# Kernel optimization log

Measured on AMD Instinct MI355X. Metric: run time of the kernel, lower is better.

## Reference

```python
import jax, jax.numpy as jnp
import numpy as np

B, N, FD = 2, 50000, 13
E = 250000
M, H = 128, 128          # message_dim, hidden_dim
EDGE_IN = 2 * FD + 8     # 34
NODE_IN = FD + 2 * M     # 269


def _mlp(x, w1, b1, w2, b2):
    return jnp.tanh(x @ w1 + b1) @ w2 + b2


def setup_inputs() -> dict:
    root = jax.random.key(0)
    k = lambda i: jax.random.fold_in(root, i)

    def lin(i, din, dout):
        w = jax.random.normal(k(i), (din, dout), jnp.float32) * np.float32(1.0 / np.sqrt(din))
        b = jax.random.normal(k(i + 100), (dout,), jnp.float32) * np.float32(0.01)
        return w, b

    ew1, eb1 = lin(1, EDGE_IN, H); ew2, eb2 = lin(2, H, M)      # mlp_edge
    ww1, wb1 = lin(3, EDGE_IN, H); ww2, wb2 = lin(4, H, 1)      # mlp_weight
    xw1, xb1 = lin(5, EDGE_IN, H); xw2, xb2 = lin(6, H, M)      # mlp_edge_world
    yw1, yb1 = lin(7, EDGE_IN, H); yw2, yb2 = lin(8, H, 1)      # mlp_weight_world
    nw1, nb1 = lin(9, NODE_IN, H); nw2, nb2 = lin(10, H, FD)    # mlp_node

    z_h = jax.random.normal(k(20), (B, N, FD), jnp.float32)
    edge_hh = jax.random.randint(k(21), (B, 2, E), 0, N, jnp.int32)
    edge_world = jax.random.randint(k(22), (B, 2, E), 0, N, jnp.int32)
    return dict(z_h=z_h, edge_hh=edge_hh, edge_world=edge_world,
                ew1=ew1, eb1=eb1, ew2=ew2, eb2=eb2,
                ww1=ww1, wb1=wb1, ww2=ww2, wb2=wb2,
                xw1=xw1, xb1=xb1, xw2=xw2, xb2=xb2,
                yw1=yw1, yb1=yb1, yw2=yw2, yb2=yb2,
                nw1=nw1, nb1=nb1, nw2=nw2, nb2=nb2)


def _edge_features(z, s, t):
    # z: (N, FD); s, t: (E,)
    pos, vel = z[:, 0:3], z[:, 3:6]
    diff = pos[s] - pos[t]                               # (E, 3)
    dist = jnp.sum(diff * diff, axis=-1, keepdims=True)  # (E, 1) squared distance
    vxc = jnp.cross(vel[s], vel[t])                      # (E, 3)
    vxn = jnp.linalg.norm(vxc, axis=-1, keepdims=True)   # (E, 1)
    return jnp.concatenate([diff, dist, vxc, vxn], axis=-1)  # (E, 8)


def reference(z_h, edge_hh, edge_world,
              ew1, eb1, ew2, eb2, ww1, wb1, ww2, wb2,
              xw1, xb1, xw2, xb2, yw1, yb1, yw2, yb2,
              nw1, nb1, nw2, nb2):
    n_nodes = z_h.shape[1]

    def per_batch(z, e_hh, e_w):
        # normal edges
        s, t = e_hh[0], e_hh[1]
        inp = jnp.concatenate([z[s], z[t], _edge_features(z, s, t)], axis=-1)  # (E, 34)
        m = _mlp(inp, ew1, eb1, ew2, eb2)                                       # (E, M)
        w = jax.nn.sigmoid(_mlp(inp, ww1, wb1, ww2, wb2))                       # (E, 1)
        agg_h = jnp.zeros((n_nodes, M), z.dtype).at[t].add(w * m)
        # world edges
        sw, tw = e_w[0], e_w[1]
        inpw = jnp.concatenate([z[sw], z[tw], _edge_features(z, sw, tw)], axis=-1)
        mw = _mlp(inpw, xw1, xb1, xw2, xb2)
        ww_ = jax.nn.sigmoid(_mlp(inpw, yw1, yb1, yw2, yb2))
        agg_w = jnp.zeros((n_nodes, M), z.dtype).at[tw].add(ww_ * mw)
        return agg_h, agg_w

    m_agg_h, m_agg_w = jax.vmap(per_batch)(z_h, edge_hh, edge_world)  # (B, N, M) each
    input_node = jnp.concatenate([z_h, m_agg_h, m_agg_w], axis=-1)    # (B, N, 269)
    delta_z_h = _mlp(input_node, nw1, nb1, nw2, nb2)                  # (B, N, 13)
    return delta_z_h
```

## Files before the change

### kernel.cpp

```cpp
#include <hip/hip_runtime.h>
#include <hip/hip_bf16.h>

#define B_   2
#define N_   50000
#define FD_  13
#define E_   250000
#define M_   128
#define H_   128

typedef __attribute__((ext_vector_type(8))) short  short8;
typedef __attribute__((ext_vector_type(8))) __bf16 bf16x8;
typedef __attribute__((ext_vector_type(4))) float  f32x4;
typedef __attribute__((ext_vector_type(4))) unsigned int uint4v;
typedef __attribute__((ext_vector_type(8))) unsigned short ushort8;

#define AGG_BYTES  (4ull * N_ * 128 * 4)
#define HIST_BYTES (4ull * N_ * 4)
#define SORT_BYTES (4ull * E_ * 4)
#define OFF_EW1 0u
#define OFF_WW1 8192u
#define OFF_EW2 16384u
#define OFF_XW1 32768u
#define OFF_YW1 40960u
#define OFF_XW2 49152u
#define OFF_NW1 65536u
#define OFF_NW2 102400u

__device__ __forceinline__ float bf2f(unsigned short u) {
    unsigned int v = ((unsigned int)u) << 16;
    return __builtin_bit_cast(float, v);
}
__device__ __forceinline__ unsigned short f2bf(float f) {
    __bf16 h = (__bf16)f;
    return __builtin_bit_cast(unsigned short, h);
}
__device__ __forceinline__ float tanh_fast(float x) {
    float e = __expf(x + x);
    float r = __builtin_amdgcn_rcpf(e + 1.0f);
    return __builtin_fmaf(-2.0f, r, 1.0f);
}
__device__ __forceinline__ float sigmoid_fast(float x) {
    return __builtin_amdgcn_rcpf(1.0f + __expf(-x));
}
__device__ __forceinline__ f32x4 mfma16(short8 a, short8 b, f32x4 c) {
    return __builtin_amdgcn_mfma_f32_16x16x32_bf16(
        __builtin_bit_cast(bf16x8, a), __builtin_bit_cast(bf16x8, b), c, 0, 0, 0);
}

__global__ void prep_kernel(const float* __restrict__ ew1, const float* __restrict__ ww1,
                            const float* __restrict__ ew2, const float* __restrict__ xw1,
                            const float* __restrict__ yw1, const float* __restrict__ xw2,
                            const float* __restrict__ nw1, const float* __restrict__ nw2,
                            unsigned short* __restrict__ fb, uint4v* __restrict__ hist4) {
    int m = blockIdx.y, f = blockIdx.x, l = threadIdx.x;
    {
        unsigned int flat = ((unsigned int)m * gridDim.x + (unsigned int)f) * 64u + (unsigned int)l;
        const uint4v zv = {0u, 0u, 0u, 0u};
        for (unsigned int i = flat; i < 50000u; i += gridDim.x * gridDim.y * 64u)
            hist4[i] = zv;
    }
    const float* src; int K, Nn, KS; unsigned int off;
    switch (m) {
        case 0: src = ew1; K = 34;  Nn = 128; KS = 2; off = OFF_EW1; break;
        case 1: src = ww1; K = 34;  Nn = 128; KS = 2; off = OFF_WW1; break;
        case 2: src = ew2; K = 128; Nn = 128; KS = 4; off = OFF_EW2; break;
        case 3: src = xw1; K = 34;  Nn = 128; KS = 2; off = OFF_XW1; break;
        case 4: src = yw1; K = 34;  Nn = 128; KS = 2; off = OFF_YW1; break;
        case 5: src = xw2; K = 128; Nn = 128; KS = 4; off = OFF_XW2; break;
        case 6: src = nw1; K = 269; Nn = 128; KS = 9; off = OFF_NW1; break;
        default: src = nw2; K = 128; Nn = 13; KS = 4; off = OFF_NW2; break;
    }
    int NT = (Nn + 15) / 16;
    if (f >= KS * NT) return;
    int ks = f / NT, nt = f % NT;
    int n = nt * 16 + (l & 15);
    unsigned short* dst = fb + off + ((unsigned int)f * 64u + (unsigned int)l) * 8u;
    #pragma unroll
    for (int j = 0; j < 8; j++) {
        int k = ks * 32 + ((l >> 4) * 8) + j;
        int kk = k; bool valid = (k < K) && (n < Nn);
        if (m == 6) {
            if (k < 256)      kk = k + 13;
            else if (k < 269) kk = k - 256;
            else              valid = false;
            valid = valid && (n < Nn);
        }
        dst[j] = valid ? f2bf(src[kk * Nn + n]) : (unsigned short)0;
    }
}

__global__ void hist_kernel(const int* __restrict__ ehh, const int* __restrict__ eww,
                            int* __restrict__ hist) {
    int p = blockIdx.y, idx = blockIdx.x * 256 + threadIdx.x;
    if (idx >= E_) return;
    const int* eg = ((p >> 1) ? eww : ehh) + (size_t)(p & 1) * 2 * E_;
    atomicAdd(&hist[p * N_ + eg[E_ + idx]], 1);
}

__global__ void scan_kernel(int* __restrict__ hist) {
    __shared__ int part[1024];
    const int p = blockIdx.x, tid = threadIdx.x;
    int* h = hist + p * N_;
    const int lo = tid * 52;
    int cnt = N_ - lo; if (cnt < 0) cnt = 0; if (cnt > 52) cnt = 52;
    int v[52];
    int sum = 0;
    if (cnt == 52) {
        const int4* src = (const int4*)(h + lo);
        #pragma unroll
        for (int i = 0; i < 13; i++) {
            int4 t = src[i];
            v[4*i] = t.x; v[4*i+1] = t.y; v[4*i+2] = t.z; v[4*i+3] = t.w;
        }
        #pragma unroll
        for (int i = 0; i < 52; i++) sum += v[i];
    } else {
        for (int i = 0; i < cnt; i++) sum += h[lo + i];
    }
    part[tid] = sum;
    __syncthreads();
    for (int off = 1; off < 1024; off <<= 1) {
        int t = (tid >= off) ? part[tid - off] : 0;
        __syncthreads();
        part[tid] += t;
        __syncthreads();
    }
    int excl = (tid == 0) ? 0 : part[tid - 1];
    if (cnt == 52) {
        int4* dst = (int4*)(h + lo);
        #pragma unroll
        for (int i = 0; i < 13; i++) {
            int4 o;
            o.x = excl; excl += v[4*i];
            o.y = excl; excl += v[4*i+1];
            o.z = excl; excl += v[4*i+2];
            o.w = excl; excl += v[4*i+3];
            dst[i] = o;
        }
    } else {
        for (int i = 0; i < cnt; i++) { int t = h[lo + i]; h[lo + i] = excl; excl += t; }
    }
}

__global__ void scatter_kernel(const int* __restrict__ ehh, const int* __restrict__ eww,
                               int* __restrict__ hist, unsigned int* __restrict__ sorted,
                               uint4v* __restrict__ agg4) {
    int p = blockIdx.y, idx = blockIdx.x * 256 + threadIdx.x;
    {
        unsigned int flat = ((unsigned int)p * gridDim.x + (unsigned int)blockIdx.x) * 256u
                          + (unsigned int)threadIdx.x;
        const unsigned int nthr = gridDim.x * gridDim.y * 256u;
        const uint4v zv = {0u, 0u, 0u, 0u};
        for (unsigned int i = flat; i < 6400000u; i += nthr) agg4[i] = zv;
    }
    if (idx >= E_) return;
    const int* eg = ((p >> 1) ? eww : ehh) + (size_t)(p & 1) * 2 * E_;
    int s = eg[idx];
    int t = eg[E_ + idx];
    int pos = atomicAdd(&hist[p * N_ + t], 1);
    sorted[(size_t)p * E_ + pos] = (unsigned int)s | ((unsigned int)t << 16);
}

__launch_bounds__(256, 3)
__global__ void edge_kernel_agg(const float* __restrict__ z,
                                const unsigned int* __restrict__ sorted,
                                const unsigned short* __restrict__ fb,
                                float* __restrict__ agg,
                                const float* __restrict__ eb1, const float* __restrict__ wb1,
                                const float* __restrict__ ww2, const float* __restrict__ wb2,
                                const float* __restrict__ eb2,
                                const float* __restrict__ xb1, const float* __restrict__ yb1,
                                const float* __restrict__ yw2, const float* __restrict__ yb2,
                                const float* __restrict__ xb2) {
    __shared__ alignas(16) unsigned short Abuf[128][48];
    __shared__ alignas(16) unsigned short Hbuf[128][136];
    __shared__ float w_acc[128];
    __shared__ int   tgt_s[128];

    const int tid  = threadIdx.x;
    const int lane = tid & 63, wv = tid >> 6, quad = lane >> 4, c = lane & 15;
    const int pass = blockIdx.y, b = pass & 1, set = pass >> 1;
    const int ebase = blockIdx.x * 128;

    const float* zb = z + (size_t)b * N_ * FD_;
    float* aggp = agg + (size_t)pass * N_ * 128;

    const short8* Fm1 = (const short8*)(fb + (set ? OFF_XW1 : OFF_EW1));
    const short8* Fw1 = (const short8*)(fb + (set ? OFF_YW1 : OFF_WW1));
    const short8* Fm2 = (const short8*)(fb + (set ? OFF_XW2 : OFF_EW2));
    const float* B1m = set ? xb1 : eb1;
    const float* B1w = set ? yb1 : wb1;
    const float* B2m = set ? xb2 : eb2;
    const float* Wv2 = set ? yw2 : ww2;
    const float wbias = (set ? yb2 : wb2)[0];

    const int nt0 = wv * 2;
    short8 bm[2][2], bw[2][2], b2f[2][4];
    float bias1m[2], bias1w[2], bias2m[2], w2v[2];
    #pragma unroll
    for (int i = 0; i < 2; i++) {
        int nt = nt0 + i, n = nt * 16 + c;
        #pragma unroll
        for (int ks = 0; ks < 2; ks++) { bm[i][ks] = Fm1[(ks * 8 + nt) * 64 + lane];
                                         bw[i][ks] = Fw1[(ks * 8 + nt) * 64 + lane]; }
        #pragma unroll
        for (int ks = 0; ks < 4; ks++) { b2f[i][ks] = Fm2[(ks * 8 + nt) * 64 + lane]; }
        bias1m[i] = B1m[n]; bias1w[i] = B1w[n];
        bias2m[i] = B2m[n]; w2v[i] = Wv2[n];
    }

    if (tid < 128) {
        const int e = tid;
        const int prt = e >> 4, pqd = (e >> 2) & 3, prr = e & 3;
        const int wpos = pqd * 32 + prt * 4 + prr;
        int sp = ebase + wpos;
        const bool valid = (sp < E_);
        if (!valid) sp = E_ - 1;
        unsigned int st = sorted[(size_t)pass * E_ + sp];
        int s = (int)(st & 0xffffu), t = (int)(st >> 16);
        tgt_s[e] = valid ? t : -1;
        w_acc[e] = 0.0f;
        const float* zs = zb + (size_t)s * 13;
        const float* zt = zb + (size_t)t * 13;
        float fs[13], ft[13];
        __builtin_memcpy(fs, zs, 13 * sizeof(float));
        __builtin_memcpy(ft, zt, 13 * sizeof(float));
        float d0 = fs[0] - ft[0], d1 = fs[1] - ft[1], d2 = fs[2] - ft[2];
        float dist = d0 * d0 + d1 * d1 + d2 * d2;
        float c0 = fs[4] * ft[5] - fs[5] * ft[4];
        float c1 = fs[5] * ft[3] - fs[3] * ft[5];
        float c2 = fs[3] * ft[4] - fs[4] * ft[3];
        float vxn = sqrtf(c0 * c0 + c1 * c1 + c2 * c2);
        unsigned short row[40];
        #pragma unroll
        for (int j = 0; j < 13; j++) { row[j] = f2bf(fs[j]); row[13 + j] = f2bf(ft[j]); }
        row[26] = f2bf(d0); row[27] = f2bf(d1); row[28] = f2bf(d2); row[29] = f2bf(dist);
        row[30] = f2bf(c0); row[31] = f2bf(c1); row[32] = f2bf(c2); row[33] = f2bf(vxn);
        #pragma unroll
        for (int j = 34; j < 40; j++) row[j] = 0;
        #pragma unroll
        for (int v = 0; v < 5; v++) {
            short8 sv;
            #pragma unroll
            for (int j = 0; j < 8; j++) sv[j] = (short)row[v * 8 + j];
            *((short8*)&Abuf[e][v * 8]) = sv;
        }
    }
    __syncthreads();

    #pragma unroll 1
    for (int rt = 0; rt < 8; rt++) {
        const unsigned short* ar = &Abuf[rt * 16 + c][0];
        short8 a0 = *((const short8*)(ar + quad * 8));
        short8 a1 = {};
        if (quad == 0) a1 = *((const short8*)(ar + 32));
        float wpart[4] = {0.f, 0.f, 0.f, 0.f};
        #pragma unroll
        for (int i = 0; i < 2; i++) {
            f32x4 accm = {bias1m[i], bias1m[i], bias1m[i], bias1m[i]};
            f32x4 accw = {bias1w[i], bias1w[i], bias1w[i], bias1w[i]};
            accm = mfma16(a0, bm[i][0], accm);
            accm = mfma16(a1, bm[i][1], accm);
            accw = mfma16(a0, bw[i][0], accw);
            accw = mfma16(a1, bw[i][1], accw);
            int n = (nt0 + i) * 16 + c;
            #pragma unroll
            for (int r = 0; r < 4; r++) {
                Hbuf[rt * 16 + quad * 4 + r][n] = f2bf(tanh_fast(accm[r]));
                wpart[r] += tanh_fast(accw[r]) * w2v[i];
            }
        }
        #pragma unroll
        for (int r = 0; r < 4; r++) {
            float v = wpart[r];
            v += __shfl_xor(v, 1); v += __shfl_xor(v, 2);
            v += __shfl_xor(v, 4); v += __shfl_xor(v, 8);
            if (c == r) atomicAdd(&w_acc[rt * 16 + quad * 4 + r], v);
        }
    }
    __syncthreads();
    if (tid < 128) w_acc[tid] = sigmoid_fast(w_acc[tid] + wbias);
    __syncthreads();

    {
        const int n0 = nt0 * 16 + c;
        const int n1 = n0 + 16;
        int   tp = -1;
        float va0 = 0.f, va1 = 0.f;
        bool  from_start = true;
        #pragma unroll 1
        for (int rt = 0; rt < 8; rt++) {
            const unsigned short* hr = &Hbuf[rt * 16 + c][0];
            short8 h0 = *((const short8*)(hr + quad * 8));
            short8 h1 = *((const short8*)(hr + 32 + quad * 8));
            short8 h2 = *((const short8*)(hr + 64 + quad * 8));
            short8 h3 = *((const short8*)(hr + 96 + quad * 8));
            f32x4 accA = {bias2m[0], bias2m[0], bias2m[0], bias2m[0]};
            f32x4 accB = {bias2m[1], bias2m[1], bias2m[1], bias2m[1]};
            accA = mfma16(h0, b2f[0][0], accA);
            accA = mfma16(h1, b2f[0][1], accA);
            accA = mfma16(h2, b2f[0][2], accA);
            accA = mfma16(h3, b2f[0][3], accA);
            accB = mfma16(h0, b2f[1][0], accB);
            accB = mfma16(h1, b2f[1][1], accB);
            accB = mfma16(h2, b2f[1][2], accB);
            accB = mfma16(h3, b2f[1][3], accB);
            const int elq = rt * 16 + quad * 4;
            #pragma unroll
            for (int r = 0; r < 4; r++) {
                const int row = elq + r;
                const int tg = tgt_s[row];
                const float g = w_acc[row];
                const float v0 = accA[r] * g;
                const float v1 = accB[r] * g;
                if (tg == tp) {
                    va0 += v0; va1 += v1;
                } else {
                    if (tp >= 0) {
                        float* dst = aggp + (size_t)tp * 128;
                        if (from_start) { atomicAdd(dst + n0, va0); atomicAdd(dst + n1, va1); }
                        else            { dst[n0] = va0; dst[n1] = va1; }
                    }
                    tp = tg; va0 = v0; va1 = v1;
                    from_start = (rt == 0 && r == 0);
                }
            }
        }
        if (tp >= 0) {
            float* dst = aggp + (size_t)tp * 128;
            atomicAdd(dst + n0, va0);
            atomicAdd(dst + n1, va1);
        }
    }
}

#define NODE_BLOCKS 1024
__launch_bounds__(256, 4)
__global__ void node_fused(const float* __restrict__ z,
                           const float* __restrict__ agg,
                           const unsigned short* __restrict__ fb,
                           const float* __restrict__ nb1,
                           const float* __restrict__ nb2,
                           float* __restrict__ out) {
    __shared__ alignas(16) unsigned short Abuf[2][16][296];
    __shared__ alignas(16) unsigned short Hbuf[16][136];

    const int tid  = threadIdx.x;
    const int lane = tid & 63, wv = tid >> 6, quad = lane >> 4, c = lane & 15;
    const int nl = tid >> 4, part = tid & 15;
    constexpr int NT_TILES = (B_ * N_) / 16;

    for (int j = tid; j < 2 * 16 * 19; j += 256) {
        int bufi = j / (16 * 19), jj = j % (16 * 19);
        Abuf[bufi][jj / 19][269 + jj % 19] = 0;
    }

    const short8* F1 = (const short8*)(fb + OFF_NW1);
    const short8* F2 = (const short8*)(fb + OFF_NW2);
    const int nt0 = wv * 2;
    const float b1a = nb1[nt0 * 16 + c];
    const float b1b = nb1[(nt0 + 1) * 16 + c];
    const float bias2 = (c < 13) ? nb2[c] : 0.0f;

    f32x4 pa0, pa1, pb0, pb1;
    float pz = 0.0f;

    int t = blockIdx.x;

    {
        const int g = t * 16 + nl;
        const int b = (g >= N_) ? 1 : 0;
        const int tt = g - b * N_;
        const float* ap0 = agg + ((size_t)b * N_ + tt) * 128 + part * 8;
        const float* ap1 = agg + ((size_t)(2 + b) * N_ + tt) * 128 + part * 8;
        pa0 = *(const f32x4*)(ap0); pa1 = *(const f32x4*)(ap0 + 4);
        pb0 = *(const f32x4*)(ap1); pb1 = *(const f32x4*)(ap1 + 4);
        if (tid < 208) pz = z[(size_t)(t * 16 + tid / 13) * 13 + (tid % 13)];
    }

    int buf = 0;
    for (; t < NT_TILES; t += NODE_BLOCKS) {
        const int g0 = t * 16;
        {
            ushort8 u;
            #pragma unroll
            for (int k = 0; k < 4; k++) { u[k] = f2bf(pa0[k]); u[4 + k] = f2bf(pa1[k]); }
            *((ushort8*)&Abuf[buf][nl][part * 8]) = u;
            #pragma unroll
            for (int k = 0; k < 4; k++) { u[k] = f2bf(pb0[k]); u[4 + k] = f2bf(pb1[k]); }
            *((ushort8*)&Abuf[buf][nl][128 + part * 8]) = u;
            if (tid < 208) Abuf[buf][tid / 13][256 + tid % 13] = f2bf(pz);
        }
        const int tn = t + NODE_BLOCKS;
        if (tn < NT_TILES) {
            const int g = tn * 16 + nl;
            const int b = (g >= N_) ? 1 : 0;
            const int tt = g - b * N_;
            const float* ap0 = agg + ((size_t)b * N_ + tt) * 128 + part * 8;
            const float* ap1 = agg + ((size_t)(2 + b) * N_ + tt) * 128 + part * 8;
            pa0 = *(const f32x4*)(ap0); pa1 = *(const f32x4*)(ap0 + 4);
            pb0 = *(const f32x4*)(ap1); pb1 = *(const f32x4*)(ap1 + 4);
            if (tid < 208) pz = z[(size_t)(tn * 16 + tid / 13) * 13 + (tid % 13)];
        }
        __syncthreads();

        {
            f32x4 acc0 = {b1a, b1a, b1a, b1a};
            f32x4 acc1 = {b1b, b1b, b1b, b1b};
            #pragma unroll
            for (int ks = 0; ks < 9; ks++) {
                short8 a = *((const short8*)(&Abuf[buf][c][0] + ks * 32 + quad * 8));
                acc0 = mfma16(a, F1[(ks * 8 + nt0) * 64 + lane], acc0);
                acc1 = mfma16(a, F1[(ks * 8 + nt0 + 1) * 64 + lane], acc1);
            }
            #pragma unroll
            for (int r = 0; r < 4; r++) {
                Hbuf[quad * 4 + r][nt0 * 16 + c]       = f2bf(tanh_fast(acc0[r]));
                Hbuf[quad * 4 + r][(nt0 + 1) * 16 + c] = f2bf(tanh_fast(acc1[r]));
            }
        }
        __syncthreads();

        if (wv == 0) {
            f32x4 acc = {bias2, bias2, bias2, bias2};
            #pragma unroll
            for (int ks = 0; ks < 4; ks++) {
                short8 h = *((const short8*)(&Hbuf[c][0] + ks * 32 + quad * 8));
                acc = mfma16(h, F2[ks * 64 + lane], acc);
            }
            #pragma unroll
            for (int r = 0; r < 4; r++) {
                int g = g0 + quad * 4 + r;
                if (c < 13) out[(size_t)g * 13 + c] = acc[r];
            }
        }
        buf ^= 1;
    }
}

extern "C" void kernel_launch(void* const* d_in, const int* in_sizes, int n_in,
                              void* d_out, int out_size, void* d_ws, size_t ws_size,
                              hipStream_t stream) {
    const float* z   = (const float*)d_in[0];
    const int* ehh   = (const int*)d_in[1];
    const int* eww   = (const int*)d_in[2];
    const float* ew1 = (const float*)d_in[3];
    const float* eb1 = (const float*)d_in[4];
    const float* ew2 = (const float*)d_in[5];
    const float* eb2 = (const float*)d_in[6];
    const float* ww1 = (const float*)d_in[7];
    const float* wb1 = (const float*)d_in[8];
    const float* ww2 = (const float*)d_in[9];
    const float* wb2 = (const float*)d_in[10];
    const float* xw1 = (const float*)d_in[11];
    const float* xb1 = (const float*)d_in[12];
    const float* xw2 = (const float*)d_in[13];
    const float* xb2 = (const float*)d_in[14];
    const float* yw1 = (const float*)d_in[15];
    const float* yb1 = (const float*)d_in[16];
    const float* yw2 = (const float*)d_in[17];
    const float* yb2 = (const float*)d_in[18];
    const float* nw1 = (const float*)d_in[19];
    const float* nb1 = (const float*)d_in[20];
    const float* nw2 = (const float*)d_in[21];
    const float* nb2 = (const float*)d_in[22];

    float* agg  = (float*)d_ws;
    int* hist   = (int*)((char*)d_ws + AGG_BYTES);
    unsigned int* sorted = (unsigned int*)((char*)d_ws + AGG_BYTES + HIST_BYTES);
    unsigned short* frag = (unsigned short*)((char*)d_ws + AGG_BYTES + HIST_BYTES + SORT_BYTES);

    prep_kernel<<<dim3(72, 8), 64, 0, stream>>>(ew1, ww1, ew2, xw1, yw1, xw2, nw1, nw2,
                                                frag, (uint4v*)hist);
    hist_kernel<<<dim3((E_ + 255) / 256, 4), 256, 0, stream>>>(ehh, eww, hist);
    scan_kernel<<<4, 1024, 0, stream>>>(hist);
    scatter_kernel<<<dim3((E_ + 255) / 256, 4), 256, 0, stream>>>(ehh, eww, hist, sorted,
                                                                  (uint4v*)agg);
    edge_kernel_agg<<<dim3((E_ + 127) / 128, 4), 256, 0, stream>>>(
        z, sorted, frag, agg,
        eb1, wb1, ww2, wb2, eb2,
        xb1, yb1, yw2, yb2, xb2);
    node_fused<<<NODE_BLOCKS, 256, 0, stream>>>(
        z, agg, frag, nb1, nb2, (float*)d_out);
}
```

Measured before the change: 399.9 us.

## Move agg zeroing to prep kernel, use exp2 intrinsics, raise node occupancy

```diff
diff --git a/kernel.cpp b/kernel.cpp
--- a/kernel.cpp
+++ b/kernel.cpp
@@ -35,12 +35,13 @@
     return __builtin_bit_cast(unsigned short, h);
 }
 __device__ __forceinline__ float tanh_fast(float x) {
-    float e = __expf(x + x);
+    float e = __builtin_amdgcn_exp2f(x * 2.8853900817779268f);
     float r = __builtin_amdgcn_rcpf(e + 1.0f);
     return __builtin_fmaf(-2.0f, r, 1.0f);
 }
 __device__ __forceinline__ float sigmoid_fast(float x) {
-    return __builtin_amdgcn_rcpf(1.0f + __expf(-x));
+    float e = __builtin_amdgcn_exp2f(x * -1.4426950408889634f);
+    return __builtin_amdgcn_rcpf(1.0f + e);
 }
 __device__ __forceinline__ f32x4 mfma16(short8 a, short8 b, f32x4 c) {
     return __builtin_amdgcn_mfma_f32_16x16x32_bf16(
@@ -51,14 +52,19 @@
                             const float* __restrict__ ew2, const float* __restrict__ xw1,
                             const float* __restrict__ yw1, const float* __restrict__ xw2,
                             const float* __restrict__ nw1, const float* __restrict__ nw2,
-                            unsigned short* __restrict__ fb, uint4v* __restrict__ hist4) {
-    int m = blockIdx.y, f = blockIdx.x, l = threadIdx.x;
+                            unsigned short* __restrict__ fb,
+                            uint4v* __restrict__ hist4, uint4v* __restrict__ agg4) {
+    const int m = blockIdx.y, f = blockIdx.x, tid = threadIdx.x;
     {
-        unsigned int flat = ((unsigned int)m * gridDim.x + (unsigned int)f) * 64u + (unsigned int)l;
+        const unsigned int flat = ((unsigned int)m * gridDim.x + (unsigned int)f) * 256u
+                                + (unsigned int)tid;
+        const unsigned int nthr = gridDim.x * gridDim.y * 256u;
         const uint4v zv = {0u, 0u, 0u, 0u};
-        for (unsigned int i = flat; i < 50000u; i += gridDim.x * gridDim.y * 64u)
-            hist4[i] = zv;
-    }
+        for (unsigned int i = flat; i < 6400000u; i += nthr) agg4[i] = zv;
+        for (unsigned int i = flat; i < 50000u;  i += nthr) hist4[i] = zv;
+    }
+    if (tid >= 64) return;
+    const int l = tid;
     const float* src; int K, Nn, KS; unsigned int off;
     switch (m) {
         case 0: src = ew1; K = 34;  Nn = 128; KS = 2; off = OFF_EW1; break;
@@ -143,16 +149,8 @@
 }
 
 __global__ void scatter_kernel(const int* __restrict__ ehh, const int* __restrict__ eww,
-                               int* __restrict__ hist, unsigned int* __restrict__ sorted,
-                               uint4v* __restrict__ agg4) {
+                               int* __restrict__ hist, unsigned int* __restrict__ sorted) {
     int p = blockIdx.y, idx = blockIdx.x * 256 + threadIdx.x;
-    {
-        unsigned int flat = ((unsigned int)p * gridDim.x + (unsigned int)blockIdx.x) * 256u
-                          + (unsigned int)threadIdx.x;
-        const unsigned int nthr = gridDim.x * gridDim.y * 256u;
-        const uint4v zv = {0u, 0u, 0u, 0u};
-        for (unsigned int i = flat; i < 6400000u; i += nthr) agg4[i] = zv;
-    }
     if (idx >= E_) return;
     const int* eg = ((p >> 1) ? eww : ehh) + (size_t)(p & 1) * 2 * E_;
     int s = eg[idx];
@@ -334,8 +332,8 @@
     }
 }
 
-#define NODE_BLOCKS 1024
-__launch_bounds__(256, 4)
+#define NODE_BLOCKS 1536
+__launch_bounds__(256, 6)
 __global__ void node_fused(const float* __restrict__ z,
                            const float* __restrict__ agg,
                            const unsigned short* __restrict__ fb,
@@ -366,6 +364,7 @@
     float pz = 0.0f;
 
     int t = blockIdx.x;
+    if (t >= NT_TILES) return;
 
     {
         const int g = t * 16 + nl;
@@ -470,12 +469,11 @@
     unsigned int* sorted = (unsigned int*)((char*)d_ws + AGG_BYTES + HIST_BYTES);
     unsigned short* frag = (unsigned short*)((char*)d_ws + AGG_BYTES + HIST_BYTES + SORT_BYTES);
 
-    prep_kernel<<<dim3(72, 8), 64, 0, stream>>>(ew1, ww1, ew2, xw1, yw1, xw2, nw1, nw2,
-                                                frag, (uint4v*)hist);
+    prep_kernel<<<dim3(72, 8), 256, 0, stream>>>(ew1, ww1, ew2, xw1, yw1, xw2, nw1, nw2,
+                                                 frag, (uint4v*)hist, (uint4v*)agg);
     hist_kernel<<<dim3((E_ + 255) / 256, 4), 256, 0, stream>>>(ehh, eww, hist);
     scan_kernel<<<4, 1024, 0, stream>>>(hist);
-    scatter_kernel<<<dim3((E_ + 255) / 256, 4), 256, 0, stream>>>(ehh, eww, hist, sorted,
-                                                                  (uint4v*)agg);
+    scatter_kernel<<<dim3((E_ + 255) / 256, 4), 256, 0, stream>>>(ehh, eww, hist, sorted);
     edge_kernel_agg<<<dim3((E_ + 127) / 128, 4), 256, 0, stream>>>(
         z, sorted, frag, agg,
         eb1, wb1, ww2, wb2, eb2,
```

Measured after the change: 495.1 us. +23.8%, slower.
